# Performance work log

Hardware: AMD Instinct MI355X
Metric: run time of the kernel (lower is better)

## Reference

```python
import jax, jax.numpy as jnp
import numpy as np

N_NODES = 100000
N_EDGES = 1600000
N_GRAPHS = 2000
IN_DIM, HID, OUT_DIM, N_CLS = 6, 256, 128, 60
EPS = 1e-5


def setup_inputs() -> dict:
    key = jax.random.key(0)
    ks = jax.random.split(key, 16)
    def lin(k, i, o):
        s = 1.0 / np.sqrt(i)
        k1, k2 = jax.random.split(k)
        return (jax.random.uniform(k1, (i, o), jnp.float32, -s, s),
                jax.random.uniform(k2, (o,), jnp.float32, -s, s))
    W_emb, b_emb = lin(ks[0], IN_DIM, HID)
    Wc1, bc1 = lin(ks[1], HID, HID)
    W2, b2 = lin(ks[2], HID, HID)
    Wc2, bc2 = lin(ks[3], HID, HID)
    W3, b3 = lin(ks[4], HID, OUT_DIM)
    Wcls, bcls = lin(ks[5], OUT_DIM, N_CLS)
    return {
        'node_features': jax.random.normal(ks[6], (N_NODES, IN_DIM), jnp.float32),
        'src': jax.random.randint(ks[7], (N_EDGES,), 0, N_NODES, jnp.int32),
        'dst': jax.random.randint(ks[8], (N_EDGES,), 0, N_NODES, jnp.int32),
        'graph_ids': jnp.sort(jax.random.randint(ks[9], (N_NODES,), 0, N_GRAPHS, jnp.int32)),
        'W_emb': W_emb, 'b_emb': b_emb,
        'Wc1': Wc1, 'bc1': bc1,
        'g1': jnp.ones((HID,), jnp.float32), 'be1': jnp.zeros((HID,), jnp.float32),
        'W2': W2, 'b2': b2,
        'Wc2': Wc2, 'bc2': bc2,
        'g2': jnp.ones((HID,), jnp.float32), 'be2': jnp.zeros((HID,), jnp.float32),
        'W3': W3, 'b3': b3,
        'Wcls': Wcls, 'bcls': bcls,
    }


def _graph_conv(x, W, b, src, dst, dout_isqrt, din_isqrt):
    # DGL GraphConv, norm='both': msg = x_src * dout^-1/2, sum to dst, * din^-1/2, then W, b
    m = x[src] * dout_isqrt[src][:, None]            # [E, H]
    agg = jax.ops.segment_sum(m, dst, num_segments=N_NODES)
    agg = agg * din_isqrt[:, None]
    return agg @ W + b


def _bn(h, g, b):
    # BatchNorm1d, training mode: batch stats over node dim, biased variance
    mu = jnp.mean(h, axis=0)
    var = jnp.mean(jnp.square(h - mu), axis=0)
    return (h - mu) * jax.lax.rsqrt(var + EPS) * g + b


def reference(node_features, src, dst, graph_ids, W_emb, b_emb, Wc1, bc1, g1, be1,
              W2, b2, Wc2, bc2, g2, be2, W3, b3, Wcls, bcls):
    ones_e = jnp.ones((N_EDGES,), jnp.float32)
    dout = jax.ops.segment_sum(ones_e, src, num_segments=N_NODES)
    din = jax.ops.segment_sum(ones_e, dst, num_segments=N_NODES)
    dout_isqrt = jnp.where(dout > 0, jax.lax.rsqrt(jnp.maximum(dout, 1.0)), 0.0)
    din_isqrt = jnp.where(din > 0, jax.lax.rsqrt(jnp.maximum(din, 1.0)), 0.0)

    x = node_features @ W_emb + b_emb                              # [N, H]
    h = x + _graph_conv(x, Wc1, bc1, src, dst, dout_isqrt, din_isqrt)
    h = jax.nn.relu(_bn(h, g1, be1))
    h = h @ W2 + b2
    h = x + _graph_conv(h, Wc2, bc2, src, dst, dout_isqrt, din_isqrt)
    h = jax.nn.relu(_bn(h, g2, be2))
    h = h @ W3 + b3                                                # [N, OUT_DIM]

    # dgl.mean_nodes: per-graph mean of h
    sums = jax.ops.segment_sum(h, graph_ids, num_segments=N_GRAPHS)
    cnts = jax.ops.segment_sum(jnp.ones((N_NODES,), jnp.float32), graph_ids, num_segments=N_GRAPHS)
    y = sums / jnp.maximum(cnts, 1.0)[:, None]                     # [G, OUT_DIM]
    label = y @ Wcls + bcls                                        # [G, N_CLS]
    return h, label
```

## Files before the change

kernel.cpp:

```cpp
#include <hip/hip_runtime.h>

#define NNODES 100000
#define MPAD   100032
#define NEDGES 1600000
#define NGRAPHS 2000
#define HID 256
#define OUTD 128
#define NCLS 60
#define BN_EPS 1e-5f
#define NROWBLK 1563
#define NSCANBLK 98
#define REDBLK 32
#define CHUNK 16384
#define NCHUNK 7
#define NSLICE 32
#define ESLICE 50000

typedef __attribute__((ext_vector_type(8))) short bf16x8;
typedef __attribute__((ext_vector_type(4))) float f32x4;

__device__ __forceinline__ float b2f(unsigned short b) {
    unsigned int u = ((unsigned int)b) << 16;
    return __builtin_bit_cast(float, u);
}
__device__ __forceinline__ unsigned short f2b(float f) {
    unsigned int u = __builtin_bit_cast(unsigned int, f);
    u = (u + 0x7FFFu + ((u >> 16) & 1u)) >> 16;
    return (unsigned short)u;
}

__global__ __launch_bounds__(256) void k_hist(
        const int* __restrict__ src, const int* __restrict__ dst,
        int* __restrict__ partialD, int* __restrict__ partialS,
        int* __restrict__ lrank) {
    __shared__ int h[CHUNK];
    int bid = blockIdx.x;
    bool isD = bid < NCHUNK * NSLICE;
    int id = isD ? bid : bid - NCHUNK * NSLICE;
    int c = id / NSLICE, s = id % NSLICE;
    int tid = threadIdx.x;
    for (int i = tid; i < CHUNK; i += 256) h[i] = 0;
    __syncthreads();
    int e0 = s * ESLICE;
    int lo = c * CHUNK;
    if (isD) {
#pragma unroll 4
        for (int e = e0 + tid; e < e0 + ESLICE; e += 256) {
            int d = dst[e];
            unsigned int b = (unsigned int)(d - lo);
            if (b < CHUNK) lrank[e] = atomicAdd(&h[b], 1);
        }
    } else {
#pragma unroll 4
        for (int e = e0 + tid; e < e0 + ESLICE; e += 256) {
            int d = src[e];
            unsigned int b = (unsigned int)(d - lo);
            if (b < CHUNK) atomicAdd(&h[b], 1);
        }
    }
    __syncthreads();
    int* out = (isD ? partialD : partialS) + ((size_t)c * NSLICE + s) * CHUNK;
    for (int i = tid; i < CHUNK; i += 256) out[i] = h[i];
}

__global__ __launch_bounds__(256) void k_sprefix(
        int* __restrict__ partialD, const int* __restrict__ partialS,
        int* __restrict__ din, float* __restrict__ dos, float* __restrict__ dis) {
    int g = blockIdx.x * 256 + threadIdx.x;
    int c = g >> 14, bin = g & (CHUNK - 1);
    int acc = 0;
#pragma unroll 4
    for (int s = 0; s < NSLICE; ++s) {
        size_t idx = ((size_t)c * NSLICE + s) * CHUNK + bin;
        int v = partialD[idx];
        partialD[idx] = acc;
        acc += v;
    }
    int so = 0;
#pragma unroll 4
    for (int s = 0; s < NSLICE; ++s)
        so += partialS[((size_t)c * NSLICE + s) * CHUNK + bin];
    if (g < NNODES) {
        din[g] = acc;
        dos[g] = so > 0 ? rsqrtf((float)so) : 0.f;
        dis[g] = acc > 0 ? rsqrtf((float)acc) : 0.f;
    }
}

__global__ void k_blk_sum(const int* __restrict__ din, int* __restrict__ bsum) {
    __shared__ int red[256];
    int blk = blockIdx.x, tid = threadIdx.x;
    int base = blk * 1024;
    int s = 0;
#pragma unroll
    for (int j = 0; j < 4; ++j) {
        int i = base + tid + j * 256;
        if (i < NNODES) s += din[i];
    }
    red[tid] = s;
    __syncthreads();
    for (int off = 128; off > 0; off >>= 1) {
        if (tid < off) red[tid] += red[tid + off];
        __syncthreads();
    }
    if (tid == 0) bsum[blk] = red[0];
}

__global__ void k_scan_bsum(int* __restrict__ bsum) {
    if (threadIdx.x == 0) {
        int acc = 0;
        for (int i = 0; i < NSCANBLK; ++i) { int v = bsum[i]; bsum[i] = acc; acc += v; }
    }
}

__global__ void k_scan_local(const int* __restrict__ deg, const int* __restrict__ bsum,
                             int* __restrict__ row_ptr) {
    __shared__ int buf[1024];
    int blk = blockIdx.x, tid = threadIdx.x;
    int i = blk * 1024 + tid;
    int v = (i < NNODES) ? deg[i] : 0;
    buf[tid] = v;
    __syncthreads();
    for (int off = 1; off < 1024; off <<= 1) {
        int t = (tid >= off) ? buf[tid - off] : 0;
        __syncthreads();
        buf[tid] += t;
        __syncthreads();
    }
    int inc = buf[tid] + bsum[blk];
    if (i < NNODES) row_ptr[i + 1] = inc;
    if (i == 0) row_ptr[0] = 0;
}

__global__ __launch_bounds__(256) void k_place(
        const int* __restrict__ src, const int* __restrict__ dst,
        const int* __restrict__ lrank, const int* __restrict__ row_ptr,
        const int* __restrict__ partialD, int* __restrict__ csr_e) {
    int e = blockIdx.x * 256 + threadIdx.x;
    if (e >= NEDGES) return;
    int d = dst[e];
    int s = e / ESLICE;
    int c = d >> 14, bin = d & (CHUNK - 1);
    int pos = row_ptr[d] + partialD[((size_t)c * NSLICE + s) * CHUNK + bin] + lrank[e];
    csr_e[pos] = src[e];
}

__global__ void k_prep(const float* __restrict__ nf, const float* __restrict__ dos,
                       float* __restrict__ nf7,
                       const float* __restrict__ W2, const float* __restrict__ Wc2,
                       const float* __restrict__ W3, unsigned short* __restrict__ Wt2,
                       unsigned short* __restrict__ Wtc2, unsigned short* __restrict__ Wt3,
                       const float* __restrict__ Wemb, const float* __restrict__ bemb,
                       const float* __restrict__ Wc1, float* __restrict__ M1,
                       float* __restrict__ v1) {
    int blk = blockIdx.x, tid = threadIdx.x;
    if (blk < 391) {
        int n = blk * 256 + tid;
        if (n < NNODES) {
            float w = dos[n];
            const float* p = nf + (size_t)n * 6;
            float4 lo = {p[0] * w, p[1] * w, p[2] * w, p[3] * w};
            float4 hi = {p[4] * w, p[5] * w, w, 0.f};
            float4* o = (float4*)(nf7 + (size_t)n * 8);
            o[0] = lo; o[1] = hi;
        }
    } else if (blk < 1031) {
        int idx = (blk - 391) * 256 + tid;
        if (idx < 65536) {
            int n = idx >> 8, k = idx & 255;
            Wt2[idx] = f2b(W2[k * 256 + n]);
        } else if (idx < 131072) {
            int j = idx - 65536;
            int n = j >> 8, k = j & 255;
            Wtc2[j] = f2b(Wc2[k * 256 + n]);
        } else {
            int j = idx - 131072;
            int n = j >> 8, k = j & 255;
            Wt3[j] = f2b(W3[k * 128 + n]);
        }
    } else {
        int bi = blk - 1031;
        int c = tid;
        float acc = 0.f;
        if (bi < 6) {
            for (int k = 0; k < HID; ++k) acc = fmaf(Wemb[bi * HID + k], Wc1[k * HID + c], acc);
            M1[bi * HID + c] = acc;
        } else {
            for (int k = 0; k < HID; ++k) acc = fmaf(bemb[k], Wc1[k * HID + c], acc);
            v1[c] = acc;
        }
    }
}

__global__ void k_agg6(const int* __restrict__ row_ptr, const int* __restrict__ csr_e,
                       const float* __restrict__ nf7, float* __restrict__ t7) {
    int n = blockIdx.x * blockDim.x + threadIdx.x;
    if (n >= NNODES) return;
    float a0 = 0, a1 = 0, a2 = 0, a3 = 0, a4 = 0, a5 = 0, a6 = 0;
    int s = row_ptr[n], e = row_ptr[n + 1];
    int i = s;
    for (; i + 2 <= e; i += 2) {
        const float4* p0 = (const float4*)(nf7 + (size_t)csr_e[i] * 8);
        const float4* p1 = (const float4*)(nf7 + (size_t)csr_e[i + 1] * 8);
        float4 l0 = p0[0], h0 = p0[1], l1 = p1[0], h1 = p1[1];
        a0 += l0.x; a1 += l0.y; a2 += l0.z; a3 += l0.w; a4 += h0.x; a5 += h0.y; a6 += h0.z;
        a0 += l1.x; a1 += l1.y; a2 += l1.z; a3 += l1.w; a4 += h1.x; a5 += h1.y; a6 += h1.z;
    }
    if (i < e) {
        const float4* p0 = (const float4*)(nf7 + (size_t)csr_e[i] * 8);
        float4 l0 = p0[0], h0 = p0[1];
        a0 += l0.x; a1 += l0.y; a2 += l0.z; a3 += l0.w; a4 += h0.x; a5 += h0.y; a6 += h0.z;
    }
    float4* o = (float4*)(t7 + (size_t)n * 8);
    o[0] = make_float4(a0, a1, a2, a3);
    o[1] = make_float4(a4, a5, a6, 0.f);
}

__global__ __launch_bounds__(256) void k_layer1(
    const float* __restrict__ nf, const float* __restrict__ Wemb, const float* __restrict__ bemb,
    const float* __restrict__ M1, const float* __restrict__ v1, const float* __restrict__ bc1,
    const float* __restrict__ t7, const float* __restrict__ dis,
    unsigned short* __restrict__ H, float* __restrict__ psum, float* __restrict__ psq) {
    __shared__ float s_nf[64][6];
    __shared__ float s_t7[64][8];
    __shared__ float s_r[64];
    int blk = blockIdx.x;
    int n0 = blk * 64;
    int tid = threadIdx.x;
    for (int t = tid; t < 384; t += 256) {
        int nl = t / 6, i = t % 6;
        int n = n0 + nl;
        s_nf[nl][i] = (n < NNODES) ? nf[(size_t)n * 6 + i] : 0.f;
    }
    if (tid < 128) {
        int n = n0 + tid / 2;
        if (n < NNODES)
            ((float4*)s_t7)[tid] = ((const float4*)(t7 + (size_t)n0 * 8))[tid];
        else
            ((float4*)s_t7)[tid] = make_float4(0.f, 0.f, 0.f, 0.f);
    }
    if (tid < 64) {
        int n = n0 + tid;
        s_r[tid] = (n < NNODES) ? dis[n] : 0.f;
    }
    int c = tid;
    float wc[6], mc[6];
#pragma unroll
    for (int i = 0; i < 6; ++i) { wc[i] = Wemb[i * HID + c]; mc[i] = M1[i * HID + c]; }
    float v1c = v1[c];
    float bsum = bemb[c] + bc1[c];
    __syncthreads();
    float ps = 0.f, pq = 0.f;
    int nmax = min(64, NNODES - n0);
    for (int nl = 0; nl < nmax; ++nl) {
        float nfd = 0.f, td = 0.f;
#pragma unroll
        for (int i = 0; i < 6; ++i) {
            nfd = fmaf(s_nf[nl][i], wc[i], nfd);
            td = fmaf(s_t7[nl][i], mc[i], td);
        }
        float val = nfd + s_r[nl] * (td + s_t7[nl][6] * v1c) + bsum;
        H[(size_t)(n0 + nl) * HID + c] = f2b(val);
        ps += val;
        pq = fmaf(val, val, pq);
    }
    for (int nl = nmax; nl < 64; ++nl) H[(size_t)(n0 + nl) * HID + c] = 0;
    psum[blk * HID + c] = ps;
    psq[blk * HID + c] = pq;
}

__global__ void k_bn_part(const float* __restrict__ psum, const float* __restrict__ psq,
                          double* __restrict__ tmp) {
    int c = threadIdx.x;
    int s = blockIdx.x;
    double a = 0.0, b = 0.0;
    for (int bb = s; bb < NROWBLK; bb += REDBLK) {
        a += psum[bb * HID + c];
        b += psq[bb * HID + c];
    }
    tmp[s * HID + c] = a;
    tmp[(REDBLK + s) * HID + c] = b;
}

__global__ void k_bn_final(const double* __restrict__ tmp, const float* __restrict__ g,
                           const float* __restrict__ be, float* __restrict__ scale,
                           float* __restrict__ shift) {
    int c = threadIdx.x;
    double s = 0.0, q = 0.0;
    for (int i = 0; i < REDBLK; ++i) { s += tmp[i * HID + c]; q += tmp[(REDBLK + i) * HID + c]; }
    double mu = s / (double)NNODES;
    double var = q / (double)NNODES - mu * mu;
    if (var < 0.0) var = 0.0;
    double inv = 1.0 / sqrt(var + (double)BN_EPS);
    float sc = (float)((double)g[c] * inv);
    scale[c] = sc;
    shift[c] = be[c] - (float)mu * sc;
}

template <int NC, bool ATRANS, bool XEPI, bool PART, bool OUTF32, bool RS>
__global__ __launch_bounds__(256, 2) void k_mgemm(
    const unsigned short* __restrict__ A, const unsigned short* __restrict__ Bt,
    const float* __restrict__ bias,
    const float* __restrict__ scale, const float* __restrict__ shift,
    const float* __restrict__ nf, const float* __restrict__ Wemb, const float* __restrict__ bemb,
    const float* __restrict__ rs,
    unsigned short* __restrict__ Cb, float* __restrict__ Cf,
    float* __restrict__ psum, float* __restrict__ psq) {
    __shared__ unsigned short As[64 * 256];
    __shared__ unsigned short Bs[64 * 256];
    __shared__ float sSc[HID];
    __shared__ float sSh[HID];
    __shared__ float sNf[64][6];
    __shared__ float sXW[6][HID];
    __shared__ float sRs[64];
    __shared__ float redS[2][64];
    __shared__ float redQ[2][64];

    int tid = threadIdx.x;
    int rb = blockIdx.x;
    int row0 = rb * 64;

    if (ATRANS) { sSc[tid] = scale[tid]; sSh[tid] = shift[tid]; }
    if (RS && tid < 64) {
        int n = row0 + tid;
        sRs[tid] = (n < NNODES) ? rs[n] : 0.f;
    }
    if (XEPI) {
        for (int t = tid; t < 6 * NC; t += 256) {
            int i = t / NC, cl = t % NC;
            sXW[i][cl] = Wemb[i * HID + cl];
        }
        if (tid < 64) {
            int n = row0 + tid;
#pragma unroll
            for (int i = 0; i < 6; ++i) sNf[tid][i] = (n < NNODES) ? nf[(size_t)n * 6 + i] : 0.f;
        }
    }
    if (ATRANS) __syncthreads();

#pragma unroll
    for (int i = 0; i < 8; ++i) {
        int g = i * 256 + tid;
        int row = g >> 5, kc = g & 31;
        uint4 v = *(const uint4*)(A + (size_t)(row0 + row) * 256 + kc * 8);
        if (ATRANS) {
            unsigned int w[4] = {v.x, v.y, v.z, v.w};
#pragma unroll
            for (int q = 0; q < 4; ++q) {
                int k0 = kc * 8 + q * 2;
                float f0 = b2f((unsigned short)(w[q] & 0xffffu));
                float f1 = b2f((unsigned short)(w[q] >> 16));
                f0 = fmaxf(fmaf(f0, sSc[k0], sSh[k0]), 0.f);
                f1 = fmaxf(fmaf(f1, sSc[k0 + 1], sSh[k0 + 1]), 0.f);
                w[q] = (unsigned int)f2b(f0) | ((unsigned int)f2b(f1) << 16);
            }
            v.x = w[0]; v.y = w[1]; v.z = w[2]; v.w = w[3];
        }
        int pkc = kc ^ (row & 7);
        *(uint4*)(&As[row * 256 + pkc * 8]) = v;
    }

    int w = tid >> 6, lane = tid & 63;
    int wm = w >> 1, wn = w & 1;
    int lrow = lane & 15, lk = lane >> 4;

    for (int cb = 0; cb < NC / 64; ++cb) {
        int c0 = cb * 64;
        if (cb) __syncthreads();
#pragma unroll
        for (int i = 0; i < 8; ++i) {
            int g = i * 256 + tid;
            int row = g >> 5, kc = g & 31;
            uint4 v = *(const uint4*)(Bt + (size_t)(c0 + row) * 256 + kc * 8);
            int pkc = kc ^ (row & 7);
            *(uint4*)(&Bs[row * 256 + pkc * 8]) = v;
        }
        __syncthreads();

        f32x4 acc[2][2] = {};
#pragma unroll
        for (int ks = 0; ks < 8; ++ks) {
            bf16x8 af[2], bfr[2];
#pragma unroll
            for (int fm = 0; fm < 2; ++fm) {
                int r = wm * 32 + fm * 16 + lrow;
                int kc = ks * 4 + lk;
                af[fm] = *(const bf16x8*)(&As[r * 256 + (kc ^ (r & 7)) * 8]);
            }
#pragma unroll
            for (int fn = 0; fn < 2; ++fn) {
                int r = wn * 32 + fn * 16 + lrow;
                int kc = ks * 4 + lk;
                bfr[fn] = *(const bf16x8*)(&Bs[r * 256 + (kc ^ (r & 7)) * 8]);
            }
#pragma unroll
            for (int fm = 0; fm < 2; ++fm)
#pragma unroll
                for (int fn = 0; fn < 2; ++fn)
                    acc[fm][fn] = __builtin_amdgcn_mfma_f32_16x16x32_bf16(af[fm], bfr[fn], acc[fm][fn], 0, 0, 0);
        }

        float pS[2] = {0.f, 0.f}, pQ[2] = {0.f, 0.f};
#pragma unroll
        for (int fn = 0; fn < 2; ++fn) {
            int cl = wn * 32 + fn * 16 + lrow;
            int gc = c0 + cl;
            float bv = bias[gc];
            if (XEPI) bv += bemb[gc];
#pragma unroll
            for (int fm = 0; fm < 2; ++fm) {
#pragma unroll
                for (int r = 0; r < 4; ++r) {
                    int rl = wm * 32 + fm * 16 + lk * 4 + r;
                    int gr = row0 + rl;
                    float val = acc[fm][fn][r] + bv;
                    if (XEPI) {
#pragma unroll
                        for (int l = 0; l < 6; ++l) val = fmaf(sNf[rl][l], sXW[l][gc], val);
                    }
                    if (RS) val *= sRs[rl];
                    if (gr < NNODES) {
                        if (OUTF32) Cf[(size_t)gr * NC + gc] = val;
                        else        Cb[(size_t)gr * NC + gc] = f2b(val);
                        if (PART) { pS[fn] += val; pQ[fn] = fmaf(val, val, pQ[fn]); }
                    }
                }
            }
        }
        if (PART) {
#pragma unroll
            for (int fn = 0; fn < 2; ++fn) {
                float s = pS[fn], q = pQ[fn];
                s += __shfl_xor(s, 16); s += __shfl_xor(s, 32);
                q += __shfl_xor(q, 16); q += __shfl_xor(q, 32);
                if (lk == 0) {
                    int cl = wn * 32 + fn * 16 + lrow;
                    redS[wm][cl] = s;
                    redQ[wm][cl] = q;
                }
            }
            __syncthreads();
            if (tid < 64) {
                psum[(size_t)rb * HID + c0 + tid] = redS[0][tid] + redS[1][tid];
                psq [(size_t)rb * HID + c0 + tid] = redQ[0][tid] + redQ[1][tid];
            }
        }
    }
}

#define ADD8(vv) { \
    a[0] += b2f((unsigned short)(vv.x & 0xffffu)); \
    a[1] += b2f((unsigned short)(vv.x >> 16)); \
    a[2] += b2f((unsigned short)(vv.y & 0xffffu)); \
    a[3] += b2f((unsigned short)(vv.y >> 16)); \
    a[4] += b2f((unsigned short)(vv.z & 0xffffu)); \
    a[5] += b2f((unsigned short)(vv.z >> 16)); \
    a[6] += b2f((unsigned short)(vv.w & 0xffffu)); \
    a[7] += b2f((unsigned short)(vv.w >> 16)); }

__global__ __launch_bounds__(256) void k_agg(const int* __restrict__ row_ptr,
                                             const int* __restrict__ csr_e,
                                             const unsigned short* __restrict__ X,
                                             const float* __restrict__ dis,
                                             unsigned short* __restrict__ out) {
    int wid = threadIdx.x >> 6, lane = threadIdx.x & 63;
    int half = lane >> 5, l32 = lane & 31;
    int n = blockIdx.x * 4 + wid;
    if (n >= NNODES) return;
    int s = row_ptr[n], e = row_ptr[n + 1];
    float a[8] = {0.f, 0.f, 0.f, 0.f, 0.f, 0.f, 0.f, 0.f};
    int i = s;
    for (; i + 8 <= e; i += 8) {
        int s0 = csr_e[i + half];
        int s1 = csr_e[i + 2 + half];
        int s2 = csr_e[i + 4 + half];
        int s3 = csr_e[i + 6 + half];
        uint4 v0 = ((const uint4*)(X + (size_t)s0 * HID))[l32];
        uint4 v1 = ((const uint4*)(X + (size_t)s1 * HID))[l32];
        uint4 v2 = ((const uint4*)(X + (size_t)s2 * HID))[l32];
        uint4 v3 = ((const uint4*)(X + (size_t)s3 * HID))[l32];
        ADD8(v0) ADD8(v1) ADD8(v2) ADD8(v3)
    }
    for (; i + 2 <= e; i += 2) {
        int s0 = csr_e[i + half];
        uint4 v0 = ((const uint4*)(X + (size_t)s0 * HID))[l32];
        ADD8(v0)
    }
    if (i < e && half == 0) {
        int s0 = csr_e[i];
        uint4 v0 = ((const uint4*)(X + (size_t)s0 * HID))[l32];
        ADD8(v0)
    }
#pragma unroll
    for (int j = 0; j < 8; ++j) a[j] += __shfl_xor(a[j], 32);
    if (half == 0) {
        float r = dis[n];
        uint4 o;
        o.x = (unsigned)f2b(a[0] * r) | ((unsigned)f2b(a[1] * r) << 16);
        o.y = (unsigned)f2b(a[2] * r) | ((unsigned)f2b(a[3] * r) << 16);
        o.z = (unsigned)f2b(a[4] * r) | ((unsigned)f2b(a[5] * r) << 16);
        o.w = (unsigned)f2b(a[6] * r) | ((unsigned)f2b(a[7] * r) << 16);
        ((uint4*)(out + (size_t)n * HID))[l32] = o;
    }
}

__global__ __launch_bounds__(128) void k_mean_label(const float* __restrict__ Hout,
                                                    const int* __restrict__ gids,
                                                    const float* __restrict__ Wcls,
                                                    const float* __restrict__ bcls,
                                                    float* __restrict__ lab) {
    int g = blockIdx.x;
    int c = threadIdx.x;
    int lo = 0, hi = NNODES;
    while (lo < hi) { int mid = (lo + hi) >> 1; if (gids[mid] < g) lo = mid + 1; else hi = mid; }
    int s = lo;
    hi = NNODES;
    while (lo < hi) { int mid = (lo + hi) >> 1; if (gids[mid] < g + 1) lo = mid + 1; else hi = mid; }
    int e = lo;
    float acc = 0.f;
    for (int n = s; n < e; ++n) acc += Hout[(size_t)n * OUTD + c];
    int cnt = e - s;
    float y = acc / (float)max(cnt, 1);
    __shared__ float ys[OUTD];
    ys[c] = y;
    __syncthreads();
    if (c < NCLS) {
        float a = bcls[c];
        for (int k = 0; k < OUTD; ++k) a = fmaf(ys[k], Wcls[k * NCLS + c], a);
        lab[(size_t)g * NCLS + c] = a;
    }
}

extern "C" void kernel_launch(void* const* d_in, const int* in_sizes, int n_in,
                              void* d_out, int out_size, void* d_ws, size_t ws_size,
                              hipStream_t stream) {
    const float* nf   = (const float*)d_in[0];
    const int*   src  = (const int*)d_in[1];
    const int*   dst  = (const int*)d_in[2];
    const int*   gids = (const int*)d_in[3];
    const float* Wemb = (const float*)d_in[4];
    const float* bemb = (const float*)d_in[5];
    const float* Wc1  = (const float*)d_in[6];
    const float* bc1  = (const float*)d_in[7];
    const float* g1   = (const float*)d_in[8];
    const float* be1  = (const float*)d_in[9];
    const float* W2   = (const float*)d_in[10];
    const float* b2   = (const float*)d_in[11];
    const float* Wc2  = (const float*)d_in[12];
    const float* bc2  = (const float*)d_in[13];
    const float* g2   = (const float*)d_in[14];
    const float* be2  = (const float*)d_in[15];
    const float* W3   = (const float*)d_in[16];
    const float* b3   = (const float*)d_in[17];
    const float* Wcls = (const float*)d_in[18];
    const float* bcls = (const float*)d_in[19];

    float* out_h   = (float*)d_out;
    float* out_lab = out_h + (size_t)NNODES * OUTD;

    float* ws = (float*)d_ws;
    size_t off = 0;
    auto take = [&](size_t n) { float* p = ws + off; off += (n + 63) & ~(size_t)63; return p; };
    unsigned short* actA = (unsigned short*)take((size_t)MPAD * HID / 2);
    unsigned short* actB = (unsigned short*)take((size_t)MPAD * HID / 2);
    unsigned short* Wt2  = (unsigned short*)take(HID * HID / 2);
    unsigned short* Wtc2 = (unsigned short*)take(HID * HID / 2);
    unsigned short* Wt3  = (unsigned short*)take(OUTD * HID / 2);
    float* dout_is = take(NNODES);
    float* din_is  = take(NNODES);
    int*   row_ptr = (int*)take(NNODES + 1);
    int*   din     = (int*)take(NNODES);
    int*   csr_e   = (int*)take(NEDGES);
    float* t7      = take((size_t)MPAD * 8);
    float* nf7_ps  = take(800320);
    float* M1      = take(6 * HID);
    float* v1      = take(HID);
    float* scale1  = take(HID);
    float* shift1  = take(HID);
    float* scale2  = take(HID);
    float* shift2  = take(HID);
    int*   bsum    = (int*)take(128);
    double* bn_tmp = (double*)take(2 * 2 * REDBLK * HID);

    int*   partialD = (int*)actA;
    int*   partialS = partialD + (size_t)NCHUNK * NSLICE * CHUNK;
    int*   lrank    = (int*)actB;
    float* nf7      = nf7_ps;
    float* psum     = nf7_ps;
    float* psq      = nf7_ps + 400128;

    k_hist<<<2 * NCHUNK * NSLICE, 256, 0, stream>>>(src, dst, partialD, partialS, lrank);
    k_sprefix<<<NCHUNK * CHUNK / 256, 256, 0, stream>>>(partialD, partialS, din,
                                                        dout_is, din_is);
    k_blk_sum<<<NSCANBLK, 256, 0, stream>>>(din, bsum);
    k_scan_bsum<<<1, 64, 0, stream>>>(bsum);
    k_scan_local<<<NSCANBLK, 1024, 0, stream>>>(din, bsum, row_ptr);
    k_place<<<(NEDGES + 255) / 256, 256, 0, stream>>>(src, dst, lrank, row_ptr,
                                                      partialD, csr_e);
    k_prep<<<1038, 256, 0, stream>>>(nf, dout_is, nf7, W2, Wc2, W3, Wt2, Wtc2, Wt3,
                                     Wemb, bemb, Wc1, M1, v1);
    k_agg6<<<(NNODES + 255) / 256, 256, 0, stream>>>(row_ptr, csr_e, nf7, t7);
    k_layer1<<<NROWBLK, 256, 0, stream>>>(nf, Wemb, bemb, M1, v1, bc1, t7, din_is,
                                          actA, psum, psq);
    k_bn_part<<<REDBLK, 256, 0, stream>>>(psum, psq, bn_tmp);
    k_bn_final<<<1, 256, 0, stream>>>(bn_tmp, g1, be1, scale1, shift1);
    k_mgemm<HID, true, false, false, false, true><<<NROWBLK, 256, 0, stream>>>(
        actA, Wt2, b2, scale1, shift1, nullptr, nullptr, nullptr, dout_is,
        actB, nullptr, nullptr, nullptr);
    k_agg<<<NNODES / 4, 256, 0, stream>>>(row_ptr, csr_e, actB, din_is, actA);
    k_mgemm<HID, false, true, true, false, false><<<NROWBLK, 256, 0, stream>>>(
        actA, Wtc2, bc2, nullptr, nullptr, nf, Wemb, bemb, nullptr,
        actB, nullptr, psum, psq);
    k_bn_part<<<REDBLK, 256, 0, stream>>>(psum, psq, bn_tmp);
    k_bn_final<<<1, 256, 0, stream>>>(bn_tmp, g2, be2, scale2, shift2);
    k_mgemm<OUTD, true, false, false, true, false><<<NROWBLK, 256, 0, stream>>>(
        actB, Wt3, b3, scale2, shift2, nullptr, nullptr, nullptr, nullptr,
        nullptr, out_h, nullptr, nullptr);
    k_mean_label<<<NGRAPHS, OUTD, 0, stream>>>(out_h, gids, Wcls, bcls, out_lab);
}
```

Measured before the change: 683.5 us.

## Fuse neighbor aggregation into second conv GEMM's A-tile load

Removes the standalone k_agg kernel and instead has the conv2 GEMM gather and sum neighbor rows via CSR directly into its shared-memory A tile, scaled by din^-1/2. This avoids writing and re-reading the aggregated intermediate in global memory and saves a launch. The trade-off is that the latency-bound gather now runs inside a 2-blocks-per-CU GEMM with each wave processing 16 rows serially, reducing memory-level parallelism; output buffers are swapped accordingly.

```diff
diff --git a/kernel.cpp b/kernel.cpp
--- a/kernel.cpp
+++ b/kernel.cpp
@@ -297,13 +297,25 @@
     shift[c] = be[c] - (float)mu * sc;
 }
 
-template <int NC, bool ATRANS, bool XEPI, bool PART, bool OUTF32, bool RS>
+#define ADD8(vv) { \
+    a[0] += b2f((unsigned short)(vv.x & 0xffffu)); \
+    a[1] += b2f((unsigned short)(vv.x >> 16)); \
+    a[2] += b2f((unsigned short)(vv.y & 0xffffu)); \
+    a[3] += b2f((unsigned short)(vv.y >> 16)); \
+    a[4] += b2f((unsigned short)(vv.z & 0xffffu)); \
+    a[5] += b2f((unsigned short)(vv.z >> 16)); \
+    a[6] += b2f((unsigned short)(vv.w & 0xffffu)); \
+    a[7] += b2f((unsigned short)(vv.w >> 16)); }
+
+template <int NC, bool ATRANS, bool XEPI, bool PART, bool OUTF32, bool RS, bool GATHER>
 __global__ __launch_bounds__(256, 2) void k_mgemm(
     const unsigned short* __restrict__ A, const unsigned short* __restrict__ Bt,
     const float* __restrict__ bias,
     const float* __restrict__ scale, const float* __restrict__ shift,
     const float* __restrict__ nf, const float* __restrict__ Wemb, const float* __restrict__ bemb,
     const float* __restrict__ rs,
+    const int* __restrict__ row_ptr, const int* __restrict__ csr_e,
+    const unsigned short* __restrict__ GX, const float* __restrict__ gdis,
     unsigned short* __restrict__ Cb, float* __restrict__ Cf,
     float* __restrict__ psum, float* __restrict__ psq) {
     __shared__ unsigned short As[64 * 256];
@@ -338,26 +350,73 @@
     }
     if (ATRANS) __syncthreads();
 
-#pragma unroll
-    for (int i = 0; i < 8; ++i) {
-        int g = i * 256 + tid;
-        int row = g >> 5, kc = g & 31;
-        uint4 v = *(const uint4*)(A + (size_t)(row0 + row) * 256 + kc * 8);
-        if (ATRANS) {
-            unsigned int w[4] = {v.x, v.y, v.z, v.w};
-#pragma unroll
-            for (int q = 0; q < 4; ++q) {
-                int k0 = kc * 8 + q * 2;
-                float f0 = b2f((unsigned short)(w[q] & 0xffffu));
-                float f1 = b2f((unsigned short)(w[q] >> 16));
-                f0 = fmaxf(fmaf(f0, sSc[k0], sSh[k0]), 0.f);
-                f1 = fmaxf(fmaf(f1, sSc[k0 + 1], sSh[k0 + 1]), 0.f);
-                w[q] = (unsigned int)f2b(f0) | ((unsigned int)f2b(f1) << 16);
-            }
-            v.x = w[0]; v.y = w[1]; v.z = w[2]; v.w = w[3];
-        }
-        int pkc = kc ^ (row & 7);
-        *(uint4*)(&As[row * 256 + pkc * 8]) = v;
+    if (GATHER) {
+        int wv = tid >> 6, lane = tid & 63;
+        int ghalf = lane >> 5, l32 = lane & 31;
+        for (int rr = 0; rr < 16; ++rr) {
+            int rl = wv * 16 + rr;
+            int n = row0 + rl;
+            float a[8] = {0.f, 0.f, 0.f, 0.f, 0.f, 0.f, 0.f, 0.f};
+            float r = 0.f;
+            if (n < NNODES) {
+                r = gdis[n];
+                int s = row_ptr[n], e = row_ptr[n + 1];
+                int i = s;
+                for (; i + 8 <= e; i += 8) {
+                    int s0 = csr_e[i + ghalf];
+                    int s1 = csr_e[i + 2 + ghalf];
+                    int s2 = csr_e[i + 4 + ghalf];
+                    int s3 = csr_e[i + 6 + ghalf];
+                    uint4 v0 = ((const uint4*)(GX + (size_t)s0 * HID))[l32];
+                    uint4 v1 = ((const uint4*)(GX + (size_t)s1 * HID))[l32];
+                    uint4 v2 = ((const uint4*)(GX + (size_t)s2 * HID))[l32];
+                    uint4 v3 = ((const uint4*)(GX + (size_t)s3 * HID))[l32];
+                    ADD8(v0) ADD8(v1) ADD8(v2) ADD8(v3)
+                }
+                for (; i + 2 <= e; i += 2) {
+                    int s0 = csr_e[i + ghalf];
+                    uint4 v0 = ((const uint4*)(GX + (size_t)s0 * HID))[l32];
+                    ADD8(v0)
+                }
+                if (i < e && ghalf == 0) {
+                    int s0 = csr_e[i];
+                    uint4 v0 = ((const uint4*)(GX + (size_t)s0 * HID))[l32];
+                    ADD8(v0)
+                }
+            }
+#pragma unroll
+            for (int j = 0; j < 8; ++j) a[j] += __shfl_xor(a[j], 32);
+            if (ghalf == 0) {
+                uint4 o;
+                o.x = (unsigned)f2b(a[0] * r) | ((unsigned)f2b(a[1] * r) << 16);
+                o.y = (unsigned)f2b(a[2] * r) | ((unsigned)f2b(a[3] * r) << 16);
+                o.z = (unsigned)f2b(a[4] * r) | ((unsigned)f2b(a[5] * r) << 16);
+                o.w = (unsigned)f2b(a[6] * r) | ((unsigned)f2b(a[7] * r) << 16);
+                *(uint4*)(&As[rl * 256 + (l32 ^ (rl & 7)) * 8]) = o;
+            }
+        }
+    } else {
+#pragma unroll
+        for (int i = 0; i < 8; ++i) {
+            int g = i * 256 + tid;
+            int row = g >> 5, kc = g & 31;
+            uint4 v = *(const uint4*)(A + (size_t)(row0 + row) * 256 + kc * 8);
+            if (ATRANS) {
+                unsigned int w[4] = {v.x, v.y, v.z, v.w};
+#pragma unroll
+                for (int q = 0; q < 4; ++q) {
+                    int k0 = kc * 8 + q * 2;
+                    float f0 = b2f((unsigned short)(w[q] & 0xffffu));
+                    float f1 = b2f((unsigned short)(w[q] >> 16));
+                    f0 = fmaxf(fmaf(f0, sSc[k0], sSh[k0]), 0.f);
+                    f1 = fmaxf(fmaf(f1, sSc[k0 + 1], sSh[k0 + 1]), 0.f);
+                    w[q] = (unsigned int)f2b(f0) | ((unsigned int)f2b(f1) << 16);
+                }
+                v.x = w[0]; v.y = w[1]; v.z = w[2]; v.w = w[3];
+            }
+            int pkc = kc ^ (row & 7);
+            *(uint4*)(&As[row * 256 + pkc * 8]) = v;
+        }
     }
 
     int w = tid >> 6, lane = tid & 63;
@@ -445,62 +504,6 @@
                 psq [(size_t)rb * HID + c0 + tid] = redQ[0][tid] + redQ[1][tid];
             }
         }
-    }
-}
-
-#define ADD8(vv) { \
-    a[0] += b2f((unsigned short)(vv.x & 0xffffu)); \
-    a[1] += b2f((unsigned short)(vv.x >> 16)); \
-    a[2] += b2f((unsigned short)(vv.y & 0xffffu)); \
-    a[3] += b2f((unsigned short)(vv.y >> 16)); \
-    a[4] += b2f((unsigned short)(vv.z & 0xffffu)); \
-    a[5] += b2f((unsigned short)(vv.z >> 16)); \
-    a[6] += b2f((unsigned short)(vv.w & 0xffffu)); \
-    a[7] += b2f((unsigned short)(vv.w >> 16)); }
-
-__global__ __launch_bounds__(256) void k_agg(const int* __restrict__ row_ptr,
-                                             const int* __restrict__ csr_e,
-                                             const unsigned short* __restrict__ X,
-                                             const float* __restrict__ dis,
-                                             unsigned short* __restrict__ out) {
-    int wid = threadIdx.x >> 6, lane = threadIdx.x & 63;
-    int half = lane >> 5, l32 = lane & 31;
-    int n = blockIdx.x * 4 + wid;
-    if (n >= NNODES) return;
-    int s = row_ptr[n], e = row_ptr[n + 1];
-    float a[8] = {0.f, 0.f, 0.f, 0.f, 0.f, 0.f, 0.f, 0.f};
-    int i = s;
-    for (; i + 8 <= e; i += 8) {
-        int s0 = csr_e[i + half];
-        int s1 = csr_e[i + 2 + half];
-        int s2 = csr_e[i + 4 + half];
-        int s3 = csr_e[i + 6 + half];
-        uint4 v0 = ((const uint4*)(X + (size_t)s0 * HID))[l32];
-        uint4 v1 = ((const uint4*)(X + (size_t)s1 * HID))[l32];
-        uint4 v2 = ((const uint4*)(X + (size_t)s2 * HID))[l32];
-        uint4 v3 = ((const uint4*)(X + (size_t)s3 * HID))[l32];
-        ADD8(v0) ADD8(v1) ADD8(v2) ADD8(v3)
-    }
-    for (; i + 2 <= e; i += 2) {
-        int s0 = csr_e[i + half];
-        uint4 v0 = ((const uint4*)(X + (size_t)s0 * HID))[l32];
-        ADD8(v0)
-    }
-    if (i < e && half == 0) {
-        int s0 = csr_e[i];
-        uint4 v0 = ((const uint4*)(X + (size_t)s0 * HID))[l32];
-        ADD8(v0)
-    }
-#pragma unroll
-    for (int j = 0; j < 8; ++j) a[j] += __shfl_xor(a[j], 32);
-    if (half == 0) {
-        float r = dis[n];
-        uint4 o;
-        o.x = (unsigned)f2b(a[0] * r) | ((unsigned)f2b(a[1] * r) << 16);
-        o.y = (unsigned)f2b(a[2] * r) | ((unsigned)f2b(a[3] * r) << 16);
-        o.z = (unsigned)f2b(a[4] * r) | ((unsigned)f2b(a[5] * r) << 16);
-        o.w = (unsigned)f2b(a[6] * r) | ((unsigned)f2b(a[7] * r) << 16);
-        ((uint4*)(out + (size_t)n * HID))[l32] = o;
     }
 }
 
@@ -604,17 +607,19 @@
                                           actA, psum, psq);
     k_bn_part<<<REDBLK, 256, 0, stream>>>(psum, psq, bn_tmp);
     k_bn_final<<<1, 256, 0, stream>>>(bn_tmp, g1, be1, scale1, shift1);
-    k_mgemm<HID, true, false, false, false, true><<<NROWBLK, 256, 0, stream>>>(
+    k_mgemm<HID, true, false, false, false, true, false><<<NROWBLK, 256, 0, stream>>>(
         actA, Wt2, b2, scale1, shift1, nullptr, nullptr, nullptr, dout_is,
+        nullptr, nullptr, nullptr, nullptr,
         actB, nullptr, nullptr, nullptr);
-    k_agg<<<NNODES / 4, 256, 0, stream>>>(row_ptr, csr_e, actB, din_is, actA);
-    k_mgemm<HID, false, true, true, false, false><<<NROWBLK, 256, 0, stream>>>(
-        actA, Wtc2, bc2, nullptr, nullptr, nf, Wemb, bemb, nullptr,
-        actB, nullptr, psum, psq);
+    k_mgemm<HID, false, true, true, false, false, true><<<NROWBLK, 256, 0, stream>>>(
+        nullptr, Wtc2, bc2, nullptr, nullptr, nf, Wemb, bemb, nullptr,
+        row_ptr, csr_e, actB, din_is,
+        actA, nullptr, psum, psq);
     k_bn_part<<<REDBLK, 256, 0, stream>>>(psum, psq, bn_tmp);
     k_bn_final<<<1, 256, 0, stream>>>(bn_tmp, g2, be2, scale2, shift2);
-    k_mgemm<OUTD, true, false, false, true, false><<<NROWBLK, 256, 0, stream>>>(
-        actB, Wt3, b3, scale2, shift2, nullptr, nullptr, nullptr, nullptr,
+    k_mgemm<OUTD, true, false, false, true, false, false><<<NROWBLK, 256, 0, stream>>>(
+        actA, Wt3, b3, scale2, shift2, nullptr, nullptr, nullptr, nullptr,
+        nullptr, nullptr, nullptr, nullptr,
         nullptr, out_h, nullptr, nullptr);
     k_mean_label<<<NGRAPHS, OUTD, 0, stream>>>(out_h, gids, Wcls, bcls, out_lab);
 }
```

Measured after the change: 729.0 us. 6.7% more time.
